# Performance work log

Measured on AMD Instinct MI355X. Metric: run time of the kernel, lower is better.

The kernel has to match this reference:

```python
import jax, jax.numpy as jnp
import numpy as np
from jax.scipy.special import erf, erfinv

N_OBS = 8192   # number of observations
N_LOC = 2048   # number of spatial locations (q)


def setup_inputs() -> dict:
    key = jax.random.key(0)
    k1, k2, k3, k4 = jax.random.split(key, 4)
    # random 2-D coordinates -> symmetric pairwise squared-distance matrix (zero diag)
    coords = jax.random.uniform(k1, (N_LOC, 2), dtype=jnp.float32) * 10.0
    dist_matrix = jnp.sum((coords[:, None, :] - coords[None, :, :]) ** 2, axis=-1)  # [q,q]
    Z_idx = jax.random.randint(k2, (N_OBS,), 0, N_LOC)                              # location id per obs
    y_true = jax.random.normal(k3, (N_OBS, 1), dtype=jnp.float32)
    y_pred = jax.random.normal(k4, (N_OBS, 1), dtype=jnp.float32) * 0.5
    return {
        "y_true": y_true,
        "y_pred": y_pred,
        "Z_idx": Z_idx,
        "dist_matrix": dist_matrix,
        "sig2e": jnp.array([1.0], dtype=jnp.float32),
        "sig2bs": jnp.array([0.5], dtype=jnp.float32),
        "lengthscale": jnp.array([2.0], dtype=jnp.float32),
    }


def _inverse_gaussian_cdf(u):
    # tf.math.erfinv(2*clip(u,1e-5,1-1e-5)-1) * sqrt(2)
    return erfinv(2.0 * jnp.clip(u, 1e-5, 1.0 - 1e-5) - 1.0) * jnp.sqrt(2.0)


def reference(y_true, y_pred, Z_idx, dist_matrix, sig2e, sig2bs, lengthscale):
    N = y_true.shape[0]
    q = dist_matrix.shape[0]
    dt = y_true.dtype
    # getD: exponential distance kernel over locations  D = sig2b * exp(-M / (2*ell))
    D = sig2bs[0] * jnp.exp(-dist_matrix / (2.0 * lengthscale[0]))          # [q,q]
    # getZ: dense one-hot design matrix (sparse.to_dense of SparseTensor of ones)
    Z = jax.nn.one_hot(Z_idx, q, dtype=dt)                                   # [N,q]
    # V_batch: V = Z D Z' + sig2e * I
    V = Z @ (D @ Z.T) + sig2e[0] * jnp.eye(N, dtype=dt)                      # [N,N]
    sd = jnp.sqrt(jnp.diagonal(V))                                           # sd_sqrt_V
    R = V / (sd[:, None] * sd[None, :])                                      # correlation matrix
    # Gaussian marginal: sig2 = sig2e + sig2b (diag of V)
    sig2 = sig2e[0] + sig2bs[0]
    resid = y_true - y_pred                                                  # [N,1]
    # distribution.cdf_batch: standard normal CDF of resid / sqrt(sig2)
    u = 0.5 * (erf(resid / jnp.sqrt(2.0 * sig2)) + 1.0)
    m = _inverse_gaussian_cdf(u)                                             # [N,1]
    # distribution.sum_log_pdf_batch: sum of Gaussian log-pdf
    sum_log_pdf = jnp.sum(-0.5 * jnp.log(2.0 * jnp.pi * sig2) - resid ** 2 / (2.0 * sig2))
    # solve + logdet via a single Cholesky of the correlation matrix
    L = jnp.linalg.cholesky(R)
    V_inv_m = jax.scipy.linalg.cho_solve((L, True), m)                       # R^{-1} m
    logdet = 2.0 * jnp.sum(jnp.log(jnp.diagonal(L)))                         # logdet(V) - 2*sum(log sd)
    mV_invm = m.T @ V_inv_m                                                  # [1,1]
    mtm = m.T @ m                                                            # [1,1]
    total_loss = 0.5 * logdet + 0.5 * mV_invm - 0.5 * mtm + 0.5 * sum_log_pdf
    return total_loss  # [1,1]
```

## Files before the change

kernel.cpp:

```cpp
#include <hip/hip_runtime.h>
#include <math.h>

#define Q 2048
#define NOBS 8192
#define NSTEPS 32

__device__ __forceinline__ float rl(float v, int l) {
  return __int_as_float(__builtin_amdgcn_readlane(__float_as_int(v), l));
}

__device__ __forceinline__ float block_sum256(float v, volatile float* red) {
  int tid = threadIdx.x;
#pragma unroll
  for (int o = 32; o > 0; o >>= 1) v += __shfl_down(v, o);
  __syncthreads();
  if ((tid & 63) == 0) red[tid >> 6] = v;
  __syncthreads();
  return red[0] + red[1] + red[2] + red[3];
}

__device__ __forceinline__ float chol64_reg(float rr[64], int lane) {
  float dv = 1.0f;
#pragma unroll
  for (int j = 0; j < 64; ++j) {
    float vjj = rl(rr[j], j);
    float invd = rsqrtf(vjj);
    float lij = rr[j] * invd;
    rr[j] = lij;
    if (lane == j) dv = lij;
#pragma unroll
    for (int k = j + 1; k < 64; ++k) rr[k] -= lij * rl(lij, k);
  }
  return dv;
}

__global__ __launch_bounds__(256) void obs_kernel(
    const float* __restrict__ yt, const float* __restrict__ yp,
    const int* __restrict__ zidx, const float* __restrict__ s2e_p,
    const float* __restrict__ s2b_p, float* __restrict__ t,
    int* __restrict__ cnt, float* __restrict__ scal) {
  __shared__ float red[4];
  int i = blockIdx.x * 256 + threadIdx.x;
  float s2e = s2e_p[0], s2b = s2b_p[0];
  float sig2 = s2e + s2b;
  float r = yt[i] - yp[i];
  float e = erff(r * rsqrtf(2.0f * sig2));
  float u = 0.5f * (e + 1.0f);
  u = fminf(fmaxf(u, 1e-5f), 1.0f - 1e-5f);
  float m = erfinvf(2.0f * u - 1.0f) * 1.4142135623730951f;
  float slp = -0.5f * logf(2.0f * 3.14159265358979f * sig2) - r * r / (2.0f * sig2);
  int z = zidx[i];
  atomicAdd(&t[z], m);
  atomicAdd(&cnt[z], 1);
  float s1 = block_sum256(slp, red);
  float s2 = block_sum256(m * m, red);
  if (threadIdx.x == 0) {
    atomicAdd(&scal[0], s1);
    atomicAdd(&scal[1], s2);
  }
}

__global__ __launch_bounds__(256) void build_G(
    const float* __restrict__ dist, const float* __restrict__ s2e_p,
    const float* __restrict__ s2b_p, const float* __restrict__ ell_p,
    const int* __restrict__ cnt, float* __restrict__ G) {
  int idx = blockIdx.x * 256 + threadIdx.x;
  int j = idx >> 11;
  int k = idx & (Q - 1);
  float s2e = s2e_p[0], s2b = s2b_p[0], ell = ell_p[0];
  float sig2 = s2e + s2b;
  float a = (s2b / sig2) * expf(-dist[idx] / (2.0f * ell));
  float g = sqrtf((float)cnt[j] * (float)cnt[k]) * a;
  if (j == k) g += s2e / sig2;
  G[idx] = g;
}

__global__ __launch_bounds__(256) void matvec_kernel(
    const float* __restrict__ dist, const float* __restrict__ s2e_p,
    const float* __restrict__ s2b_p, const float* __restrict__ ell_p,
    const int* __restrict__ cnt, const float* __restrict__ t,
    float* __restrict__ z, float* __restrict__ scal) {
  __shared__ float red[4];
  int j = blockIdx.x;
  float s2e = s2e_p[0], s2b = s2b_p[0], ell = ell_p[0];
  float sig2 = s2e + s2b;
  float inv2ell = 1.0f / (2.0f * ell);
  float s = 0.0f;
  const float* drow = dist + (size_t)j * Q;
  for (int k = threadIdx.x; k < Q; k += 256) s += expf(-drow[k] * inv2ell) * t[k];
  float tot = block_sum256(s, red);
  if (threadIdx.x == 0) {
    float wj = (s2b / sig2) * tot;
    z[j] = sqrtf((float)cnt[j]) * wj;
    atomicAdd(&scal[2], t[j] * wj);
  }
}

__global__ __launch_bounds__(64, 1) void potrf_first(
    const float* __restrict__ G, float* __restrict__ dstage,
    float* __restrict__ scal) {
  int lane = threadIdx.x;
  float rr[64];
  const float* row = G + (size_t)lane * Q;
#pragma unroll
  for (int k4 = 0; k4 < 16; ++k4) {
    float4 v = *(const float4*)(row + k4 * 4);
    rr[k4 * 4 + 0] = v.x; rr[k4 * 4 + 1] = v.y;
    rr[k4 * 4 + 2] = v.z; rr[k4 * 4 + 3] = v.w;
  }
  float dv = chol64_reg(rr, lane);
#pragma unroll
  for (int k4 = 0; k4 < 16; ++k4) {
    float4 st;
    st.x = rr[k4 * 4 + 0]; st.y = rr[k4 * 4 + 1];
    st.z = rr[k4 * 4 + 2]; st.w = rr[k4 * 4 + 3];
    *(float4*)(dstage + lane * 64 + k4 * 4) = st;
  }
  float lg = logf(dv);
#pragma unroll
  for (int o = 32; o > 0; o >>= 1) lg += __shfl_down(lg, o);
  if (lane == 0) atomicAdd(&scal[3], lg);
}

__global__ __launch_bounds__(256) void trsm_step(
    float* __restrict__ G, float* __restrict__ z,
    const float* __restrict__ dstage, int j0, int Rtot) {
  __shared__ float shA[64 * 65];
  int tid = threadIdx.x;
#pragma unroll
  for (int it = 0; it < 4; ++it) {
    int idx = it * 256 + tid;
    int r = idx >> 4, c = (idx & 15) * 4;
    float4 v = *(const float4*)(dstage + r * 64 + c);
    shA[r * 65 + c + 0] = v.x; shA[r * 65 + c + 1] = v.y;
    shA[r * 65 + c + 2] = v.z; shA[r * 65 + c + 3] = v.w;
  }
  __syncthreads();
  int lane = tid & 63, wv = tid >> 6;
  int ri = blockIdx.x * 4 + wv;
  if (ri >= Rtot) return;
  int r = j0 + 64 + ri;
  float* grow = (r < Q) ? (G + (size_t)r * Q + j0) : (z + j0);
  float a = grow[lane];
  float myinv = 1.0f / shA[lane * 65 + lane];
#pragma unroll
  for (int p = 0; p < 64; ++p) {
    float xp = rl(a, p) * rl(myinv, p);
    if (lane > p) a -= xp * shA[lane * 65 + p];
  }
  grow[lane] = a * myinv;
}

__device__ __forceinline__ void syrk_tile(float* __restrict__ G, int j0,
                                          int R0, int C0, float* shA,
                                          float* shB) {
  int tid = threadIdx.x;
#pragma unroll
  for (int it = 0; it < 4; ++it) {
    int idx = it * 256 + tid;
    int r = idx >> 4, c4 = (idx & 15) * 4;
    float4 v = *(const float4*)(G + (size_t)(R0 + r) * Q + j0 + c4);
    shA[(c4 + 0) * 68 + r] = v.x; shA[(c4 + 1) * 68 + r] = v.y;
    shA[(c4 + 2) * 68 + r] = v.z; shA[(c4 + 3) * 68 + r] = v.w;
    float4 u = *(const float4*)(G + (size_t)(C0 + r) * Q + j0 + c4);
    shB[(c4 + 0) * 68 + r] = u.x; shB[(c4 + 1) * 68 + r] = u.y;
    shB[(c4 + 2) * 68 + r] = u.z; shB[(c4 + 3) * 68 + r] = u.w;
  }
  __syncthreads();
  int tx = tid & 15, ty = tid >> 4;
  float acc[4][4] = {{0.f}};
  for (int p = 0; p < 64; ++p) {
    float4 a4 = *(const float4*)&shA[p * 68 + ty * 4];
    float4 b4 = *(const float4*)&shB[p * 68 + tx * 4];
    float av[4] = {a4.x, a4.y, a4.z, a4.w};
    float bv[4] = {b4.x, b4.y, b4.z, b4.w};
#pragma unroll
    for (int i = 0; i < 4; ++i)
#pragma unroll
      for (int jj = 0; jj < 4; ++jj) acc[i][jj] += av[i] * bv[jj];
  }
#pragma unroll
  for (int i = 0; i < 4; ++i) {
    float* gp = G + (size_t)(R0 + ty * 4 + i) * Q + C0 + tx * 4;
    float4 g = *(const float4*)gp;
    g.x -= acc[i][0]; g.y -= acc[i][1];
    g.z -= acc[i][2]; g.w -= acc[i][3];
    *(float4*)gp = g;
  }
}

__global__ __launch_bounds__(256, 1) void syrk_step(
    float* __restrict__ G, float* __restrict__ z, float* __restrict__ dstage,
    float* __restrict__ scal, int j0, int ntri) {
  __shared__ __align__(16) float shA[64 * 68];
  __shared__ __align__(16) float shB[64 * 68];
  __shared__ float z1s[64];
  int tid = threadIdx.x;
  int bx = blockIdx.x;

  if (bx == 0) {
    int D0 = j0 + 64;
#pragma unroll
    for (int it = 0; it < 4; ++it) {
      int idx = it * 256 + tid;
      int r2 = idx >> 4, c4 = (idx & 15) * 4;
      float4 v = *(const float4*)(G + (size_t)(D0 + r2) * Q + j0 + c4);
      shA[(c4 + 0) * 68 + r2] = v.x; shA[(c4 + 1) * 68 + r2] = v.y;
      shA[(c4 + 2) * 68 + r2] = v.z; shA[(c4 + 3) * 68 + r2] = v.w;
    }
    __syncthreads();
    int tx = tid & 15, ty = tid >> 4;
    float acc[4][4] = {{0.f}};
    for (int p = 0; p < 64; ++p) {
      float4 a4 = *(const float4*)&shA[p * 68 + ty * 4];
      float4 b4 = *(const float4*)&shA[p * 68 + tx * 4];
      float av[4] = {a4.x, a4.y, a4.z, a4.w};
      float bv[4] = {b4.x, b4.y, b4.z, b4.w};
#pragma unroll
      for (int i = 0; i < 4; ++i)
#pragma unroll
        for (int jj = 0; jj < 4; ++jj) acc[i][jj] += av[i] * bv[jj];
    }
#pragma unroll
    for (int i = 0; i < 4; ++i) {
      const float* gp = G + (size_t)(D0 + ty * 4 + i) * Q + D0 + tx * 4;
      float4 g = *(const float4*)gp;
      float4 o;
      o.x = g.x - acc[i][0]; o.y = g.y - acc[i][1];
      o.z = g.z - acc[i][2]; o.w = g.w - acc[i][3];
      *(float4*)&shB[(ty * 4 + i) * 68 + tx * 4] = o;
    }
    __syncthreads();
    if (tid < 64) {
      int lane = tid;
      float rr[64];
#pragma unroll
      for (int k4 = 0; k4 < 16; ++k4) {
        float4 v = *(const float4*)&shB[lane * 68 + k4 * 4];
        rr[k4 * 4 + 0] = v.x; rr[k4 * 4 + 1] = v.y;
        rr[k4 * 4 + 2] = v.z; rr[k4 * 4 + 3] = v.w;
      }
      __builtin_amdgcn_s_setprio(1);
      float dv = chol64_reg(rr, lane);
      __builtin_amdgcn_s_setprio(0);
#pragma unroll
      for (int k4 = 0; k4 < 16; ++k4) {
        float4 st;
        st.x = rr[k4 * 4 + 0]; st.y = rr[k4 * 4 + 1];
        st.z = rr[k4 * 4 + 2]; st.w = rr[k4 * 4 + 3];
        *(float4*)(dstage + lane * 64 + k4 * 4) = st;
      }
      float lg = logf(dv);
#pragma unroll
      for (int o = 32; o > 0; o >>= 1) lg += __shfl_down(lg, o);
      if (lane == 0) atomicAdd(&scal[3], lg);
    }
  } else if (bx < ntri) {
    int job = bx;
    int bi = (int)((sqrtf(8.0f * (float)job + 1.0f) - 1.0f) * 0.5f);
    while ((bi + 1) * (bi + 2) / 2 <= job) ++bi;
    while (bi * (bi + 1) / 2 > job) --bi;
    int bk = job - bi * (bi + 1) / 2;
    syrk_tile(G, j0, j0 + 64 + bi * 64, j0 + 64 + bk * 64, shA, shB);
  } else {
    int bk = bx - ntri;
    int C0 = j0 + 64 + bk * 64;
    if (tid < 64) z1s[tid] = z[j0 + tid];
    __syncthreads();
    int rw = tid >> 2, part = tid & 3;
    const float* Lr = G + (size_t)(C0 + rw) * Q + j0;
    float ssum = 0.f;
    for (int p = part; p < 64; p += 4) ssum += Lr[p] * z1s[p];
    ssum += __shfl_down(ssum, 2);
    ssum += __shfl_down(ssum, 1);
    if (part == 0) z[C0 + rw] -= ssum;
  }
}

__global__ __launch_bounds__(256) void final_assemble(
    const float* __restrict__ z, const float* __restrict__ scal,
    const float* __restrict__ s2e_p, const float* __restrict__ s2b_p,
    float* __restrict__ out) {
  __shared__ float red[4];
  int tid = threadIdx.x;
  float bv = 0.f;
  for (int i = tid; i < Q; i += 256) {
    float zi = z[i];
    bv += zi * zi;
  }
  float bvs = block_sum256(bv, red);
  if (tid == 0) {
    float s2e = s2e_p[0], s2b = s2b_p[0];
    float sig2 = s2e + s2b;
    float c = s2e / sig2;
    float slp = scal[0], mtm = scal[1];
    float tw = scal[2], sl = scal[3];
    float tty = (tw - bvs) / c;
    float mrm = (mtm - tty) / c;
    float logdetR = (float)(NOBS - Q) * logf(c) + 2.0f * sl;
    out[0] = 0.5f * logdetR + 0.5f * mrm - 0.5f * mtm + 0.5f * slp;
  }
}

extern "C" void kernel_launch(void* const* d_in, const int* in_sizes, int n_in,
                              void* d_out, int out_size, void* d_ws, size_t ws_size,
                              hipStream_t stream) {
  const float* yt   = (const float*)d_in[0];
  const float* yp   = (const float*)d_in[1];
  const int*   zidx = (const int*)d_in[2];
  const float* dist = (const float*)d_in[3];
  const float* s2e  = (const float*)d_in[4];
  const float* s2b  = (const float*)d_in[5];
  const float* ell  = (const float*)d_in[6];

  float* ws   = (float*)d_ws;
  float* G    = ws;
  float* z    = ws + (size_t)Q * Q;
  float* t    = z + Q;
  int*   cnt  = (int*)(t + Q);
  float* scal = t + 2 * Q;
  float* dstage = scal + 8;

  hipMemsetAsync(t, 0, (2 * Q + 8) * sizeof(float), stream);

  obs_kernel<<<NOBS / 256, 256, 0, stream>>>(yt, yp, zidx, s2e, s2b, t, cnt, scal);
  build_G<<<(Q * Q) / 256, 256, 0, stream>>>(dist, s2e, s2b, ell, cnt, G);
  matvec_kernel<<<Q, 256, 0, stream>>>(dist, s2e, s2b, ell, cnt, t, z, scal);

  potrf_first<<<1, 64, 0, stream>>>(G, dstage, scal);

  for (int s = 0; s < NSTEPS; ++s) {
    int j0 = s * 64;
    int ntr = Q - j0 - 64;
    int Rtot = ntr + 1;
    int nb = ntr >> 6;
    trsm_step<<<(Rtot + 3) / 4, 256, 0, stream>>>(G, z, dstage, j0, Rtot);
    if (nb > 0) {
      int ntri = nb * (nb + 1) / 2;
      syrk_step<<<ntri + nb, 256, 0, stream>>>(G, z, dstage, scal, j0, ntri);
    }
  }

  final_assemble<<<1, 256, 0, stream>>>(z, scal, s2e, s2b, (float*)d_out);
}
```

Measured before the change: 886.8 us.

## Use 128-wide panels in blocked Cholesky with 8x8 register tiles and fused G build

```diff
diff --git a/kernel.cpp b/kernel.cpp
--- a/kernel.cpp
+++ b/kernel.cpp
@@ -3,7 +3,8 @@
 
 #define Q 2048
 #define NOBS 8192
-#define NSTEPS 32
+#define BS 128
+#define NSTEPS 16
 
 __device__ __forceinline__ float rl(float v, int l) {
   return __int_as_float(__builtin_amdgcn_readlane(__float_as_int(v), l));
@@ -32,6 +33,136 @@
     for (int k = j + 1; k < 64; ++k) rr[k] -= lij * rl(lij, k);
   }
   return dv;
+}
+
+__device__ __forceinline__ void factor128_from(
+    const float* src, int sstride, float* dstage,
+    float* LT, float* Xs, float* invDs, float* scal) {
+  int tid = threadIdx.x;
+  int lane = tid & 63;
+  float lg = 0.0f;
+
+  if (tid < 64) {
+    float rr[64];
+    const float* row = src + (size_t)lane * sstride;
+#pragma unroll
+    for (int k4 = 0; k4 < 16; ++k4) {
+      float4 v = *(const float4*)(row + k4 * 4);
+      rr[k4 * 4 + 0] = v.x; rr[k4 * 4 + 1] = v.y;
+      rr[k4 * 4 + 2] = v.z; rr[k4 * 4 + 3] = v.w;
+    }
+    __builtin_amdgcn_s_setprio(1);
+    float dv = chol64_reg(rr, lane);
+    __builtin_amdgcn_s_setprio(0);
+    invDs[lane] = 1.0f / dv;
+    lg = logf(dv);
+#pragma unroll
+    for (int p = 0; p < 64; ++p)
+      LT[p * 64 + lane] = (p < lane) ? rr[p] : 0.0f;
+#pragma unroll
+    for (int k4 = 0; k4 < 16; ++k4) {
+      float4 st;
+      st.x = rr[k4 * 4 + 0]; st.y = rr[k4 * 4 + 1];
+      st.z = rr[k4 * 4 + 2]; st.w = rr[k4 * 4 + 3];
+      *(float4*)(dstage + lane * 128 + k4 * 4) = st;
+    }
+  }
+  __syncthreads();
+
+  if (tid < 64) {
+    float rr2[64];
+    const float* row = src + (size_t)(64 + lane) * sstride;
+#pragma unroll
+    for (int k4 = 0; k4 < 16; ++k4) {
+      float4 v = *(const float4*)(row + k4 * 4);
+      rr2[k4 * 4 + 0] = v.x; rr2[k4 * 4 + 1] = v.y;
+      rr2[k4 * 4 + 2] = v.z; rr2[k4 * 4 + 3] = v.w;
+    }
+    __builtin_amdgcn_s_setprio(1);
+#pragma unroll
+    for (int p = 0; p < 64; ++p) {
+      float xp = rr2[p] * invDs[p];
+      rr2[p] = xp;
+#pragma unroll
+      for (int k4 = 0; k4 < 16; ++k4) {
+        if (k4 * 4 + 3 > p) {
+          float4 l4 = *(const float4*)&LT[p * 64 + k4 * 4];
+          rr2[k4 * 4 + 0] -= xp * l4.x;
+          rr2[k4 * 4 + 1] -= xp * l4.y;
+          rr2[k4 * 4 + 2] -= xp * l4.z;
+          rr2[k4 * 4 + 3] -= xp * l4.w;
+        }
+      }
+    }
+    __builtin_amdgcn_s_setprio(0);
+#pragma unroll
+    for (int k = 0; k < 64; ++k) Xs[lane * 65 + k] = rr2[k];
+#pragma unroll
+    for (int k4 = 0; k4 < 16; ++k4) {
+      float4 st;
+      st.x = rr2[k4 * 4 + 0]; st.y = rr2[k4 * 4 + 1];
+      st.z = rr2[k4 * 4 + 2]; st.w = rr2[k4 * 4 + 3];
+      *(float4*)(dstage + (64 + lane) * 128 + k4 * 4) = st;
+    }
+  }
+  __syncthreads();
+
+  {
+    int tx = tid & 15, ty = tid >> 4;
+    float a2[4][4];
+#pragma unroll
+    for (int i = 0; i < 4; ++i)
+#pragma unroll
+      for (int j = 0; j < 4; ++j) a2[i][j] = 0.f;
+    for (int p = 0; p < 64; ++p) {
+      float xa[4], xb[4];
+#pragma unroll
+      for (int i = 0; i < 4; ++i) xa[i] = Xs[(ty * 4 + i) * 65 + p];
+#pragma unroll
+      for (int j = 0; j < 4; ++j) xb[j] = Xs[(tx * 4 + j) * 65 + p];
+#pragma unroll
+      for (int i = 0; i < 4; ++i)
+#pragma unroll
+        for (int j = 0; j < 4; ++j) a2[i][j] += xa[i] * xb[j];
+    }
+#pragma unroll
+    for (int i = 0; i < 4; ++i) {
+      int gr = 64 + ty * 4 + i;
+      const float* sp = src + (size_t)gr * sstride + 64 + tx * 4;
+      float4 s4 = *(const float4*)sp;
+      float4 o;
+      o.x = s4.x - a2[i][0]; o.y = s4.y - a2[i][1];
+      o.z = s4.z - a2[i][2]; o.w = s4.w - a2[i][3];
+      *(float4*)(dstage + gr * 128 + 64 + tx * 4) = o;
+    }
+  }
+  __syncthreads();
+  __builtin_amdgcn_fence(__ATOMIC_ACQUIRE, "workgroup");
+
+  if (tid < 64) {
+    float rr3[64];
+    const float* row = dstage + (64 + lane) * 128 + 64;
+#pragma unroll
+    for (int k4 = 0; k4 < 16; ++k4) {
+      float4 v = *(const float4*)(row + k4 * 4);
+      rr3[k4 * 4 + 0] = v.x; rr3[k4 * 4 + 1] = v.y;
+      rr3[k4 * 4 + 2] = v.z; rr3[k4 * 4 + 3] = v.w;
+    }
+    __builtin_amdgcn_s_setprio(1);
+    float dv = chol64_reg(rr3, lane);
+    __builtin_amdgcn_s_setprio(0);
+    lg += logf(dv);
+#pragma unroll
+    for (int k4 = 0; k4 < 16; ++k4) {
+      float4 st;
+      st.x = rr3[k4 * 4 + 0]; st.y = rr3[k4 * 4 + 1];
+      st.z = rr3[k4 * 4 + 2]; st.w = rr3[k4 * 4 + 3];
+      *(float4*)(dstage + (64 + lane) * 128 + 64 + k4 * 4) = st;
+    }
+#pragma unroll
+    for (int o = 32; o > 0; o >>= 1) lg += __shfl_down(lg, o);
+    if (lane == 0) atomicAdd(&scal[3], lg);
+  }
 }
 
 __global__ __launch_bounds__(256) void obs_kernel(
@@ -60,220 +191,210 @@
   }
 }
 
-__global__ __launch_bounds__(256) void build_G(
-    const float* __restrict__ dist, const float* __restrict__ s2e_p,
-    const float* __restrict__ s2b_p, const float* __restrict__ ell_p,
-    const int* __restrict__ cnt, float* __restrict__ G) {
-  int idx = blockIdx.x * 256 + threadIdx.x;
-  int j = idx >> 11;
-  int k = idx & (Q - 1);
-  float s2e = s2e_p[0], s2b = s2b_p[0], ell = ell_p[0];
-  float sig2 = s2e + s2b;
-  float a = (s2b / sig2) * expf(-dist[idx] / (2.0f * ell));
-  float g = sqrtf((float)cnt[j] * (float)cnt[k]) * a;
-  if (j == k) g += s2e / sig2;
-  G[idx] = g;
-}
-
-__global__ __launch_bounds__(256) void matvec_kernel(
+__global__ __launch_bounds__(256) void build_mv(
     const float* __restrict__ dist, const float* __restrict__ s2e_p,
     const float* __restrict__ s2b_p, const float* __restrict__ ell_p,
     const int* __restrict__ cnt, const float* __restrict__ t,
-    float* __restrict__ z, float* __restrict__ scal) {
+    float* __restrict__ G, float* __restrict__ z, float* __restrict__ scal) {
   __shared__ float red[4];
   int j = blockIdx.x;
   float s2e = s2e_p[0], s2b = s2b_p[0], ell = ell_p[0];
   float sig2 = s2e + s2b;
+  float ratio = s2b / sig2;
+  float diag = s2e / sig2;
   float inv2ell = 1.0f / (2.0f * ell);
+  float cj = (float)cnt[j];
+  const float* drow = dist + (size_t)j * Q;
+  float* grow = G + (size_t)j * Q;
   float s = 0.0f;
-  const float* drow = dist + (size_t)j * Q;
-  for (int k = threadIdx.x; k < Q; k += 256) s += expf(-drow[k] * inv2ell) * t[k];
+  for (int k = threadIdx.x; k < Q; k += 256) {
+    float e = expf(-drow[k] * inv2ell);
+    s += e * t[k];
+    float g = sqrtf(cj * (float)cnt[k]) * (ratio * e);
+    if (j == k) g += diag;
+    grow[k] = g;
+  }
   float tot = block_sum256(s, red);
   if (threadIdx.x == 0) {
-    float wj = (s2b / sig2) * tot;
-    z[j] = sqrtf((float)cnt[j]) * wj;
+    float wj = ratio * tot;
+    z[j] = sqrtf(cj) * wj;
     atomicAdd(&scal[2], t[j] * wj);
   }
 }
 
-__global__ __launch_bounds__(64, 1) void potrf_first(
+__global__ __launch_bounds__(256, 1) void potrf_first(
     const float* __restrict__ G, float* __restrict__ dstage,
     float* __restrict__ scal) {
-  int lane = threadIdx.x;
-  float rr[64];
-  const float* row = G + (size_t)lane * Q;
-#pragma unroll
-  for (int k4 = 0; k4 < 16; ++k4) {
-    float4 v = *(const float4*)(row + k4 * 4);
-    rr[k4 * 4 + 0] = v.x; rr[k4 * 4 + 1] = v.y;
-    rr[k4 * 4 + 2] = v.z; rr[k4 * 4 + 3] = v.w;
-  }
-  float dv = chol64_reg(rr, lane);
-#pragma unroll
-  for (int k4 = 0; k4 < 16; ++k4) {
-    float4 st;
-    st.x = rr[k4 * 4 + 0]; st.y = rr[k4 * 4 + 1];
-    st.z = rr[k4 * 4 + 2]; st.w = rr[k4 * 4 + 3];
-    *(float4*)(dstage + lane * 64 + k4 * 4) = st;
-  }
-  float lg = logf(dv);
-#pragma unroll
-  for (int o = 32; o > 0; o >>= 1) lg += __shfl_down(lg, o);
-  if (lane == 0) atomicAdd(&scal[3], lg);
+  __shared__ __align__(16) float smem[64 * 64 + 64 * 65];
+  __shared__ float invDs[64];
+  factor128_from(G, Q, dstage, smem, smem + 64 * 64, invDs, scal);
 }
 
 __global__ __launch_bounds__(256) void trsm_step(
     float* __restrict__ G, float* __restrict__ z,
     const float* __restrict__ dstage, int j0, int Rtot) {
-  __shared__ float shA[64 * 65];
+  __shared__ float shL[128 * 129];
   int tid = threadIdx.x;
 #pragma unroll
-  for (int it = 0; it < 4; ++it) {
+  for (int it = 0; it < 16; ++it) {
     int idx = it * 256 + tid;
-    int r = idx >> 4, c = (idx & 15) * 4;
-    float4 v = *(const float4*)(dstage + r * 64 + c);
-    shA[r * 65 + c + 0] = v.x; shA[r * 65 + c + 1] = v.y;
-    shA[r * 65 + c + 2] = v.z; shA[r * 65 + c + 3] = v.w;
+    int r = idx >> 5, c4 = (idx & 31) * 4;
+    float4 v = *(const float4*)(dstage + r * 128 + c4);
+    shL[r * 129 + c4 + 0] = v.x; shL[r * 129 + c4 + 1] = v.y;
+    shL[r * 129 + c4 + 2] = v.z; shL[r * 129 + c4 + 3] = v.w;
   }
   __syncthreads();
   int lane = tid & 63, wv = tid >> 6;
   int ri = blockIdx.x * 4 + wv;
   if (ri >= Rtot) return;
-  int r = j0 + 64 + ri;
+  int r = j0 + BS + ri;
   float* grow = (r < Q) ? (G + (size_t)r * Q + j0) : (z + j0);
-  float a = grow[lane];
-  float myinv = 1.0f / shA[lane * 65 + lane];
+  float a0 = grow[lane];
+  float a1 = grow[64 + lane];
+  float inv0 = 1.0f / shL[lane * 129 + lane];
+  float inv1 = 1.0f / shL[(64 + lane) * 129 + 64 + lane];
 #pragma unroll
   for (int p = 0; p < 64; ++p) {
-    float xp = rl(a, p) * rl(myinv, p);
-    if (lane > p) a -= xp * shA[lane * 65 + p];
-  }
-  grow[lane] = a * myinv;
-}
-
-__device__ __forceinline__ void syrk_tile(float* __restrict__ G, int j0,
-                                          int R0, int C0, float* shA,
-                                          float* shB) {
-  int tid = threadIdx.x;
-#pragma unroll
-  for (int it = 0; it < 4; ++it) {
-    int idx = it * 256 + tid;
-    int r = idx >> 4, c4 = (idx & 15) * 4;
-    float4 v = *(const float4*)(G + (size_t)(R0 + r) * Q + j0 + c4);
-    shA[(c4 + 0) * 68 + r] = v.x; shA[(c4 + 1) * 68 + r] = v.y;
-    shA[(c4 + 2) * 68 + r] = v.z; shA[(c4 + 3) * 68 + r] = v.w;
-    float4 u = *(const float4*)(G + (size_t)(C0 + r) * Q + j0 + c4);
-    shB[(c4 + 0) * 68 + r] = u.x; shB[(c4 + 1) * 68 + r] = u.y;
-    shB[(c4 + 2) * 68 + r] = u.z; shB[(c4 + 3) * 68 + r] = u.w;
-  }
-  __syncthreads();
-  int tx = tid & 15, ty = tid >> 4;
-  float acc[4][4] = {{0.f}};
+    float xp = rl(a0, p) * rl(inv0, p);
+    if (lane > p) a0 -= xp * shL[lane * 129 + p];
+    a1 -= xp * shL[(64 + lane) * 129 + p];
+  }
+#pragma unroll
   for (int p = 0; p < 64; ++p) {
-    float4 a4 = *(const float4*)&shA[p * 68 + ty * 4];
-    float4 b4 = *(const float4*)&shB[p * 68 + tx * 4];
-    float av[4] = {a4.x, a4.y, a4.z, a4.w};
-    float bv[4] = {b4.x, b4.y, b4.z, b4.w};
-#pragma unroll
-    for (int i = 0; i < 4; ++i)
-#pragma unroll
-      for (int jj = 0; jj < 4; ++jj) acc[i][jj] += av[i] * bv[jj];
-  }
-#pragma unroll
-  for (int i = 0; i < 4; ++i) {
-    float* gp = G + (size_t)(R0 + ty * 4 + i) * Q + C0 + tx * 4;
-    float4 g = *(const float4*)gp;
-    g.x -= acc[i][0]; g.y -= acc[i][1];
-    g.z -= acc[i][2]; g.w -= acc[i][3];
-    *(float4*)gp = g;
-  }
+    float xp = rl(a1, p) * rl(inv1, p);
+    if (lane > p) a1 -= xp * shL[(64 + lane) * 129 + 64 + p];
+  }
+  grow[lane] = a0 * inv0;
+  grow[64 + lane] = a1 * inv1;
 }
 
 __global__ __launch_bounds__(256, 1) void syrk_step(
     float* __restrict__ G, float* __restrict__ z, float* __restrict__ dstage,
-    float* __restrict__ scal, int j0, int ntri) {
-  __shared__ __align__(16) float shA[64 * 68];
-  __shared__ __align__(16) float shB[64 * 68];
-  __shared__ float z1s[64];
+    float* __restrict__ scal, int j0, int ntri, int nb) {
+  __shared__ __align__(16) float smem[2 * 32 * 132];
+  __shared__ float invDs[64];
+  __shared__ float z1s[128];
   int tid = threadIdx.x;
   int bx = blockIdx.x;
+  float* shA = smem;
+  float* shB = smem + 32 * 132;
+
+  if (bx >= ntri) {
+    int zj = bx - ntri;
+    int C0 = j0 + BS + zj * BS;
+    if (tid < 128) z1s[tid] = z[j0 + tid];
+    __syncthreads();
+    int rw = tid >> 1, part = tid & 1;
+    const float* Lr = G + (size_t)(C0 + rw) * Q + j0;
+    float ssum = 0.f;
+    for (int p = part; p < 128; p += 2) ssum += Lr[p] * z1s[p];
+    ssum += __shfl_down(ssum, 1);
+    if (part == 0) z[C0 + rw] -= ssum;
+    return;
+  }
+
+  int tx = tid & 15, ty = tid >> 4;
+  float acc[8][8];
+#pragma unroll
+  for (int i = 0; i < 8; ++i)
+#pragma unroll
+    for (int j = 0; j < 8; ++j) acc[i][j] = 0.f;
 
   if (bx == 0) {
-    int D0 = j0 + 64;
+    int D0 = j0 + BS;
+    for (int kk = 0; kk < 4; ++kk) {
+#pragma unroll
+      for (int it = 0; it < 4; ++it) {
+        int idx = it * 256 + tid;
+        int r = idx >> 3, c4 = (idx & 7) * 4;
+        float4 v = *(const float4*)(G + (size_t)(D0 + r) * Q + j0 + kk * 32 + c4);
+        shA[(c4 + 0) * 132 + r] = v.x; shA[(c4 + 1) * 132 + r] = v.y;
+        shA[(c4 + 2) * 132 + r] = v.z; shA[(c4 + 3) * 132 + r] = v.w;
+      }
+      __syncthreads();
+#pragma unroll
+      for (int p = 0; p < 32; ++p) {
+        float4 a0 = *(const float4*)&shA[p * 132 + ty * 8];
+        float4 a1 = *(const float4*)&shA[p * 132 + ty * 8 + 4];
+        float4 b0 = *(const float4*)&shA[p * 132 + tx * 8];
+        float4 b1 = *(const float4*)&shA[p * 132 + tx * 8 + 4];
+        float av[8] = {a0.x, a0.y, a0.z, a0.w, a1.x, a1.y, a1.z, a1.w};
+        float bv[8] = {b0.x, b0.y, b0.z, b0.w, b1.x, b1.y, b1.z, b1.w};
+#pragma unroll
+        for (int i = 0; i < 8; ++i)
+#pragma unroll
+          for (int j = 0; j < 8; ++j) acc[i][j] += av[i] * bv[j];
+      }
+      __syncthreads();
+    }
+#pragma unroll
+    for (int i = 0; i < 8; ++i) {
+      const float* gp = G + (size_t)(D0 + ty * 8 + i) * Q + D0 + tx * 8;
+      float4 g0 = *(const float4*)gp;
+      float4 g1 = *(const float4*)(gp + 4);
+      float4 o0, o1;
+      o0.x = g0.x - acc[i][0]; o0.y = g0.y - acc[i][1];
+      o0.z = g0.z - acc[i][2]; o0.w = g0.w - acc[i][3];
+      o1.x = g1.x - acc[i][4]; o1.y = g1.y - acc[i][5];
+      o1.z = g1.z - acc[i][6]; o1.w = g1.w - acc[i][7];
+      *(float4*)(dstage + (ty * 8 + i) * 128 + tx * 8) = o0;
+      *(float4*)(dstage + (ty * 8 + i) * 128 + tx * 8 + 4) = o1;
+    }
+    __syncthreads();
+    __builtin_amdgcn_fence(__ATOMIC_ACQUIRE, "workgroup");
+    factor128_from(dstage, 128, dstage, smem, smem + 64 * 64, invDs, scal);
+    return;
+  }
+
+  int job = bx;
+  int bi = (int)((sqrtf(8.0f * (float)job + 1.0f) - 1.0f) * 0.5f);
+  while ((bi + 1) * (bi + 2) / 2 <= job) ++bi;
+  while (bi * (bi + 1) / 2 > job) --bi;
+  int bk = job - bi * (bi + 1) / 2;
+  int R0 = j0 + BS + bi * BS;
+  int C0 = j0 + BS + bk * BS;
+  bool sym = (bi == bk);
+
+  for (int kk = 0; kk < 4; ++kk) {
 #pragma unroll
     for (int it = 0; it < 4; ++it) {
       int idx = it * 256 + tid;
-      int r2 = idx >> 4, c4 = (idx & 15) * 4;
-      float4 v = *(const float4*)(G + (size_t)(D0 + r2) * Q + j0 + c4);
-      shA[(c4 + 0) * 68 + r2] = v.x; shA[(c4 + 1) * 68 + r2] = v.y;
-      shA[(c4 + 2) * 68 + r2] = v.z; shA[(c4 + 3) * 68 + r2] = v.w;
+      int r = idx >> 3, c4 = (idx & 7) * 4;
+      float4 v = *(const float4*)(G + (size_t)(R0 + r) * Q + j0 + kk * 32 + c4);
+      shA[(c4 + 0) * 132 + r] = v.x; shA[(c4 + 1) * 132 + r] = v.y;
+      shA[(c4 + 2) * 132 + r] = v.z; shA[(c4 + 3) * 132 + r] = v.w;
+      if (!sym) {
+        float4 u = *(const float4*)(G + (size_t)(C0 + r) * Q + j0 + kk * 32 + c4);
+        shB[(c4 + 0) * 132 + r] = u.x; shB[(c4 + 1) * 132 + r] = u.y;
+        shB[(c4 + 2) * 132 + r] = u.z; shB[(c4 + 3) * 132 + r] = u.w;
+      }
     }
     __syncthreads();
-    int tx = tid & 15, ty = tid >> 4;
-    float acc[4][4] = {{0.f}};
-    for (int p = 0; p < 64; ++p) {
-      float4 a4 = *(const float4*)&shA[p * 68 + ty * 4];
-      float4 b4 = *(const float4*)&shA[p * 68 + tx * 4];
-      float av[4] = {a4.x, a4.y, a4.z, a4.w};
-      float bv[4] = {b4.x, b4.y, b4.z, b4.w};
-#pragma unroll
-      for (int i = 0; i < 4; ++i)
-#pragma unroll
-        for (int jj = 0; jj < 4; ++jj) acc[i][jj] += av[i] * bv[jj];
-    }
-#pragma unroll
-    for (int i = 0; i < 4; ++i) {
-      const float* gp = G + (size_t)(D0 + ty * 4 + i) * Q + D0 + tx * 4;
-      float4 g = *(const float4*)gp;
-      float4 o;
-      o.x = g.x - acc[i][0]; o.y = g.y - acc[i][1];
-      o.z = g.z - acc[i][2]; o.w = g.w - acc[i][3];
-      *(float4*)&shB[(ty * 4 + i) * 68 + tx * 4] = o;
+    const float* sB = sym ? shA : shB;
+#pragma unroll
+    for (int p = 0; p < 32; ++p) {
+      float4 a0 = *(const float4*)&shA[p * 132 + ty * 8];
+      float4 a1 = *(const float4*)&shA[p * 132 + ty * 8 + 4];
+      float4 b0 = *(const float4*)&sB[p * 132 + tx * 8];
+      float4 b1 = *(const float4*)&sB[p * 132 + tx * 8 + 4];
+      float av[8] = {a0.x, a0.y, a0.z, a0.w, a1.x, a1.y, a1.z, a1.w};
+      float bv[8] = {b0.x, b0.y, b0.z, b0.w, b1.x, b1.y, b1.z, b1.w};
+#pragma unroll
+      for (int i = 0; i < 8; ++i)
+#pragma unroll
+        for (int j = 0; j < 8; ++j) acc[i][j] += av[i] * bv[j];
     }
     __syncthreads();
-    if (tid < 64) {
-      int lane = tid;
-      float rr[64];
-#pragma unroll
-      for (int k4 = 0; k4 < 16; ++k4) {
-        float4 v = *(const float4*)&shB[lane * 68 + k4 * 4];
-        rr[k4 * 4 + 0] = v.x; rr[k4 * 4 + 1] = v.y;
-        rr[k4 * 4 + 2] = v.z; rr[k4 * 4 + 3] = v.w;
-      }
-      __builtin_amdgcn_s_setprio(1);
-      float dv = chol64_reg(rr, lane);
-      __builtin_amdgcn_s_setprio(0);
-#pragma unroll
-      for (int k4 = 0; k4 < 16; ++k4) {
-        float4 st;
-        st.x = rr[k4 * 4 + 0]; st.y = rr[k4 * 4 + 1];
-        st.z = rr[k4 * 4 + 2]; st.w = rr[k4 * 4 + 3];
-        *(float4*)(dstage + lane * 64 + k4 * 4) = st;
-      }
-      float lg = logf(dv);
-#pragma unroll
-      for (int o = 32; o > 0; o >>= 1) lg += __shfl_down(lg, o);
-      if (lane == 0) atomicAdd(&scal[3], lg);
-    }
-  } else if (bx < ntri) {
-    int job = bx;
-    int bi = (int)((sqrtf(8.0f * (float)job + 1.0f) - 1.0f) * 0.5f);
-    while ((bi + 1) * (bi + 2) / 2 <= job) ++bi;
-    while (bi * (bi + 1) / 2 > job) --bi;
-    int bk = job - bi * (bi + 1) / 2;
-    syrk_tile(G, j0, j0 + 64 + bi * 64, j0 + 64 + bk * 64, shA, shB);
-  } else {
-    int bk = bx - ntri;
-    int C0 = j0 + 64 + bk * 64;
-    if (tid < 64) z1s[tid] = z[j0 + tid];
-    __syncthreads();
-    int rw = tid >> 2, part = tid & 3;
-    const float* Lr = G + (size_t)(C0 + rw) * Q + j0;
-    float ssum = 0.f;
-    for (int p = part; p < 64; p += 4) ssum += Lr[p] * z1s[p];
-    ssum += __shfl_down(ssum, 2);
-    ssum += __shfl_down(ssum, 1);
-    if (part == 0) z[C0 + rw] -= ssum;
+  }
+#pragma unroll
+  for (int i = 0; i < 8; ++i) {
+    float* gp = G + (size_t)(R0 + ty * 8 + i) * Q + C0 + tx * 8;
+    float4 g0 = *(const float4*)gp;
+    float4 g1 = *(const float4*)(gp + 4);
+    g0.x -= acc[i][0]; g0.y -= acc[i][1]; g0.z -= acc[i][2]; g0.w -= acc[i][3];
+    g1.x -= acc[i][4]; g1.y -= acc[i][5]; g1.z -= acc[i][6]; g1.w -= acc[i][7];
+    *(float4*)gp = g0;
+    *(float4*)(gp + 4) = g1;
   }
 }
 
@@ -324,20 +445,19 @@
   hipMemsetAsync(t, 0, (2 * Q + 8) * sizeof(float), stream);
 
   obs_kernel<<<NOBS / 256, 256, 0, stream>>>(yt, yp, zidx, s2e, s2b, t, cnt, scal);
-  build_G<<<(Q * Q) / 256, 256, 0, stream>>>(dist, s2e, s2b, ell, cnt, G);
-  matvec_kernel<<<Q, 256, 0, stream>>>(dist, s2e, s2b, ell, cnt, t, z, scal);
-
-  potrf_first<<<1, 64, 0, stream>>>(G, dstage, scal);
+  build_mv<<<Q, 256, 0, stream>>>(dist, s2e, s2b, ell, cnt, t, G, z, scal);
+
+  potrf_first<<<1, 256, 0, stream>>>(G, dstage, scal);
 
   for (int s = 0; s < NSTEPS; ++s) {
-    int j0 = s * 64;
-    int ntr = Q - j0 - 64;
+    int j0 = s * BS;
+    int ntr = Q - j0 - BS;
     int Rtot = ntr + 1;
-    int nb = ntr >> 6;
+    int nb = ntr / BS;
     trsm_step<<<(Rtot + 3) / 4, 256, 0, stream>>>(G, z, dstage, j0, Rtot);
     if (nb > 0) {
       int ntri = nb * (nb + 1) / 2;
-      syrk_step<<<ntri + nb, 256, 0, stream>>>(G, z, dstage, scal, j0, ntri);
+      syrk_step<<<ntri + nb, 256, 0, stream>>>(G, z, dstage, scal, j0, ntri, nb);
     }
   }
 
```

After: 1.188 ms. 34.0% more time.

## Fuse TRSM and SYRK per step with flag-based intra-kernel dependencies

Applied to the files above, without the earlier changes.

```diff
diff --git a/kernel.cpp b/kernel.cpp
--- a/kernel.cpp
+++ b/kernel.cpp
@@ -3,7 +3,6 @@
 
 #define Q 2048
 #define NOBS 8192
-#define NSTEPS 32
 
 __device__ __forceinline__ float rl(float v, int l) {
   return __int_as_float(__builtin_amdgcn_readlane(__float_as_int(v), l));
@@ -32,6 +31,12 @@
     for (int k = j + 1; k < 64; ++k) rr[k] -= lij * rl(lij, k);
   }
   return dv;
+}
+
+__device__ __forceinline__ void wait_flag(int* f, int target) {
+  while (__hip_atomic_load(f, __ATOMIC_RELAXED, __HIP_MEMORY_SCOPE_AGENT) <
+         target)
+    __builtin_amdgcn_s_sleep(8);
 }
 
 __global__ __launch_bounds__(256) void obs_kernel(
@@ -60,45 +65,40 @@
   }
 }
 
-__global__ __launch_bounds__(256) void build_G(
-    const float* __restrict__ dist, const float* __restrict__ s2e_p,
-    const float* __restrict__ s2b_p, const float* __restrict__ ell_p,
-    const int* __restrict__ cnt, float* __restrict__ G) {
-  int idx = blockIdx.x * 256 + threadIdx.x;
-  int j = idx >> 11;
-  int k = idx & (Q - 1);
-  float s2e = s2e_p[0], s2b = s2b_p[0], ell = ell_p[0];
-  float sig2 = s2e + s2b;
-  float a = (s2b / sig2) * expf(-dist[idx] / (2.0f * ell));
-  float g = sqrtf((float)cnt[j] * (float)cnt[k]) * a;
-  if (j == k) g += s2e / sig2;
-  G[idx] = g;
-}
-
-__global__ __launch_bounds__(256) void matvec_kernel(
+__global__ __launch_bounds__(256) void build_mv(
     const float* __restrict__ dist, const float* __restrict__ s2e_p,
     const float* __restrict__ s2b_p, const float* __restrict__ ell_p,
     const int* __restrict__ cnt, const float* __restrict__ t,
-    float* __restrict__ z, float* __restrict__ scal) {
+    float* __restrict__ G, float* __restrict__ z, float* __restrict__ scal) {
   __shared__ float red[4];
   int j = blockIdx.x;
   float s2e = s2e_p[0], s2b = s2b_p[0], ell = ell_p[0];
   float sig2 = s2e + s2b;
+  float ratio = s2b / sig2;
+  float diag = s2e / sig2;
   float inv2ell = 1.0f / (2.0f * ell);
+  float cj = (float)cnt[j];
+  const float* drow = dist + (size_t)j * Q;
+  float* grow = G + (size_t)j * Q;
   float s = 0.0f;
-  const float* drow = dist + (size_t)j * Q;
-  for (int k = threadIdx.x; k < Q; k += 256) s += expf(-drow[k] * inv2ell) * t[k];
+  for (int k = threadIdx.x; k < Q; k += 256) {
+    float e = expf(-drow[k] * inv2ell);
+    s += e * t[k];
+    float g = sqrtf(cj * (float)cnt[k]) * (ratio * e);
+    if (j == k) g += diag;
+    grow[k] = g;
+  }
   float tot = block_sum256(s, red);
   if (threadIdx.x == 0) {
-    float wj = (s2b / sig2) * tot;
-    z[j] = sqrtf((float)cnt[j]) * wj;
+    float wj = ratio * tot;
+    z[j] = sqrtf(cj) * wj;
     atomicAdd(&scal[2], t[j] * wj);
   }
 }
 
 __global__ __launch_bounds__(64, 1) void potrf_first(
-    const float* __restrict__ G, float* __restrict__ dstage,
-    float* __restrict__ scal) {
+    const float* __restrict__ G, float* __restrict__ dsA,
+    float* __restrict__ z, float* __restrict__ scal) {
   int lane = threadIdx.x;
   float rr[64];
   const float* row = G + (size_t)lane * Q;
@@ -114,92 +114,85 @@
     float4 st;
     st.x = rr[k4 * 4 + 0]; st.y = rr[k4 * 4 + 1];
     st.z = rr[k4 * 4 + 2]; st.w = rr[k4 * 4 + 3];
-    *(float4*)(dstage + lane * 64 + k4 * 4) = st;
+    *(float4*)(dsA + lane * 64 + k4 * 4) = st;
   }
   float lg = logf(dv);
 #pragma unroll
   for (int o = 32; o > 0; o >>= 1) lg += __shfl_down(lg, o);
   if (lane == 0) atomicAdd(&scal[3], lg);
-}
-
-__global__ __launch_bounds__(256) void trsm_step(
-    float* __restrict__ G, float* __restrict__ z,
-    const float* __restrict__ dstage, int j0, int Rtot) {
-  __shared__ float shA[64 * 65];
-  int tid = threadIdx.x;
-#pragma unroll
-  for (int it = 0; it < 4; ++it) {
-    int idx = it * 256 + tid;
-    int r = idx >> 4, c = (idx & 15) * 4;
-    float4 v = *(const float4*)(dstage + r * 64 + c);
-    shA[r * 65 + c + 0] = v.x; shA[r * 65 + c + 1] = v.y;
-    shA[r * 65 + c + 2] = v.z; shA[r * 65 + c + 3] = v.w;
-  }
-  __syncthreads();
-  int lane = tid & 63, wv = tid >> 6;
-  int ri = blockIdx.x * 4 + wv;
-  if (ri >= Rtot) return;
-  int r = j0 + 64 + ri;
-  float* grow = (r < Q) ? (G + (size_t)r * Q + j0) : (z + j0);
-  float a = grow[lane];
-  float myinv = 1.0f / shA[lane * 65 + lane];
+  float a = z[lane];
+  float myinv = 1.0f / dv;
 #pragma unroll
   for (int p = 0; p < 64; ++p) {
     float xp = rl(a, p) * rl(myinv, p);
-    if (lane > p) a -= xp * shA[lane * 65 + p];
-  }
-  grow[lane] = a * myinv;
-}
-
-__device__ __forceinline__ void syrk_tile(float* __restrict__ G, int j0,
-                                          int R0, int C0, float* shA,
-                                          float* shB) {
-  int tid = threadIdx.x;
-#pragma unroll
-  for (int it = 0; it < 4; ++it) {
-    int idx = it * 256 + tid;
-    int r = idx >> 4, c4 = (idx & 15) * 4;
-    float4 v = *(const float4*)(G + (size_t)(R0 + r) * Q + j0 + c4);
-    shA[(c4 + 0) * 68 + r] = v.x; shA[(c4 + 1) * 68 + r] = v.y;
-    shA[(c4 + 2) * 68 + r] = v.z; shA[(c4 + 3) * 68 + r] = v.w;
-    float4 u = *(const float4*)(G + (size_t)(C0 + r) * Q + j0 + c4);
-    shB[(c4 + 0) * 68 + r] = u.x; shB[(c4 + 1) * 68 + r] = u.y;
-    shB[(c4 + 2) * 68 + r] = u.z; shB[(c4 + 3) * 68 + r] = u.w;
-  }
-  __syncthreads();
-  int tx = tid & 15, ty = tid >> 4;
-  float acc[4][4] = {{0.f}};
-  for (int p = 0; p < 64; ++p) {
-    float4 a4 = *(const float4*)&shA[p * 68 + ty * 4];
-    float4 b4 = *(const float4*)&shB[p * 68 + tx * 4];
-    float av[4] = {a4.x, a4.y, a4.z, a4.w};
-    float bv[4] = {b4.x, b4.y, b4.z, b4.w};
-#pragma unroll
-    for (int i = 0; i < 4; ++i)
-#pragma unroll
-      for (int jj = 0; jj < 4; ++jj) acc[i][jj] += av[i] * bv[jj];
-  }
-#pragma unroll
-  for (int i = 0; i < 4; ++i) {
-    float* gp = G + (size_t)(R0 + ty * 4 + i) * Q + C0 + tx * 4;
-    float4 g = *(const float4*)gp;
-    g.x -= acc[i][0]; g.y -= acc[i][1];
-    g.z -= acc[i][2]; g.w -= acc[i][3];
-    *(float4*)gp = g;
-  }
-}
-
-__global__ __launch_bounds__(256, 1) void syrk_step(
-    float* __restrict__ G, float* __restrict__ z, float* __restrict__ dstage,
-    float* __restrict__ scal, int j0, int ntri) {
-  __shared__ __align__(16) float shA[64 * 68];
-  __shared__ __align__(16) float shB[64 * 68];
+    if (lane > p) a -= xp * rr[p];
+  }
+  z[lane] = a * myinv;
+}
+
+__global__ __launch_bounds__(256, 2) void step_kernel(
+    float* __restrict__ G, float* __restrict__ z, float* __restrict__ scal,
+    const float* __restrict__ dsR, float* __restrict__ dsW,
+    int* __restrict__ flags, int j0, int ntri, int n64, int T, int mode) {
+  __shared__ __align__(16) float smem[2 * 64 * 68];
   __shared__ float z1s[64];
-  int tid = threadIdx.x;
-  int bx = blockIdx.x;
+  __shared__ float z2s[64];
+  float* shA = smem;
+  float* shB = smem + 64 * 68;
+  int tid = threadIdx.x, bx = blockIdx.x;
+  int lane = tid & 63, wv = tid >> 6;
+  int s1 = (j0 >> 6) + 1;
+  int D0 = j0 + 64;
+  int ztop = ntri + n64 - 1;
+
+  if (mode == 1 || (mode == 0 && bx >= ztop)) {
+    int t = (mode == 1) ? bx : bx - ztop;
+#pragma unroll
+    for (int it = 0; it < 4; ++it) {
+      int idx = it * 256 + tid;
+      int r = idx >> 4, c = (idx & 15) * 4;
+      float4 v = *(const float4*)(dsR + r * 64 + c);
+      shA[r * 65 + c + 0] = v.x; shA[r * 65 + c + 1] = v.y;
+      shA[r * 65 + c + 2] = v.z; shA[r * 65 + c + 3] = v.w;
+    }
+    __syncthreads();
+    int rbase = D0 + t * 16 + wv * 4;
+    float* g0 = G + (size_t)(rbase + 0) * Q + j0;
+    float* g1 = G + (size_t)(rbase + 1) * Q + j0;
+    float* g2 = G + (size_t)(rbase + 2) * Q + j0;
+    float* g3 = G + (size_t)(rbase + 3) * Q + j0;
+    float a0 = g0[lane], a1 = g1[lane], a2 = g2[lane], a3 = g3[lane];
+    float myinv = 1.0f / shA[lane * 65 + lane];
+#pragma unroll
+    for (int p = 0; p < 64; ++p) {
+      float ip = rl(myinv, p);
+      float x0 = rl(a0, p) * ip;
+      float x1 = rl(a1, p) * ip;
+      float x2 = rl(a2, p) * ip;
+      float x3 = rl(a3, p) * ip;
+      float lv = shA[lane * 65 + p];
+      if (lane > p) {
+        a0 -= x0 * lv; a1 -= x1 * lv; a2 -= x2 * lv; a3 -= x3 * lv;
+      }
+    }
+    g0[lane] = a0 * myinv; g1[lane] = a1 * myinv;
+    g2[lane] = a2 * myinv; g3[lane] = a3 * myinv;
+    __syncthreads();
+    if (tid == 0) {
+      __builtin_amdgcn_fence(__ATOMIC_RELEASE, "agent");
+      __hip_atomic_fetch_add(&flags[s1 + (t >> 2)], 1, __ATOMIC_RELAXED,
+                             __HIP_MEMORY_SCOPE_AGENT);
+    }
+    return;
+  }
 
   if (bx == 0) {
-    int D0 = j0 + 64;
+    if (tid == 0) {
+      wait_flag(&flags[s1], T);
+      __builtin_amdgcn_fence(__ATOMIC_ACQUIRE, "agent");
+    }
+    __syncthreads();
+    if (tid < 64) z1s[tid] = z[j0 + tid];
 #pragma unroll
     for (int it = 0; it < 4; ++it) {
       int idx = it * 256 + tid;
@@ -221,6 +214,14 @@
 #pragma unroll
         for (int jj = 0; jj < 4; ++jj) acc[i][jj] += av[i] * bv[jj];
     }
+    {
+      int rw = tid >> 2, part = tid & 3;
+      float ssum = 0.f;
+      for (int p = part; p < 64; p += 4) ssum += shA[p * 68 + rw] * z1s[p];
+      ssum += __shfl_down(ssum, 2);
+      ssum += __shfl_down(ssum, 1);
+      if (part == 0) z2s[rw] = z[D0 + rw] - ssum;
+    }
 #pragma unroll
     for (int i = 0; i < 4; ++i) {
       const float* gp = G + (size_t)(D0 + ty * 4 + i) * Q + D0 + tx * 4;
@@ -232,7 +233,6 @@
     }
     __syncthreads();
     if (tid < 64) {
-      int lane = tid;
       float rr[64];
 #pragma unroll
       for (int k4 = 0; k4 < 16; ++k4) {
@@ -248,25 +248,86 @@
         float4 st;
         st.x = rr[k4 * 4 + 0]; st.y = rr[k4 * 4 + 1];
         st.z = rr[k4 * 4 + 2]; st.w = rr[k4 * 4 + 3];
-        *(float4*)(dstage + lane * 64 + k4 * 4) = st;
+        *(float4*)(dsW + lane * 64 + k4 * 4) = st;
       }
       float lg = logf(dv);
 #pragma unroll
       for (int o = 32; o > 0; o >>= 1) lg += __shfl_down(lg, o);
       if (lane == 0) atomicAdd(&scal[3], lg);
-    }
-  } else if (bx < ntri) {
+      float a = z2s[lane];
+      float myinv = 1.0f / dv;
+#pragma unroll
+      for (int p = 0; p < 64; ++p) {
+        float xp = rl(a, p) * rl(myinv, p);
+        if (lane > p) a -= xp * rr[p];
+      }
+      z[D0 + lane] = a * myinv;
+    }
+    return;
+  }
+
+  if (bx < ntri) {
     int job = bx;
     int bi = (int)((sqrtf(8.0f * (float)job + 1.0f) - 1.0f) * 0.5f);
     while ((bi + 1) * (bi + 2) / 2 <= job) ++bi;
     while (bi * (bi + 1) / 2 > job) --bi;
     int bk = job - bi * (bi + 1) / 2;
-    syrk_tile(G, j0, j0 + 64 + bi * 64, j0 + 64 + bk * 64, shA, shB);
-  } else {
-    int bk = bx - ntri;
-    int C0 = j0 + 64 + bk * 64;
+    if (tid == 0) {
+      wait_flag(&flags[s1 + bi], T);
+      if (bk != bi) wait_flag(&flags[s1 + bk], T);
+      __builtin_amdgcn_fence(__ATOMIC_ACQUIRE, "agent");
+    }
+    __syncthreads();
+    int R0 = D0 + bi * 64, C0 = D0 + bk * 64;
+    bool sym = (bi == bk);
+#pragma unroll
+    for (int it = 0; it < 4; ++it) {
+      int idx = it * 256 + tid;
+      int r = idx >> 4, c4 = (idx & 15) * 4;
+      float4 v = *(const float4*)(G + (size_t)(R0 + r) * Q + j0 + c4);
+      shA[(c4 + 0) * 68 + r] = v.x; shA[(c4 + 1) * 68 + r] = v.y;
+      shA[(c4 + 2) * 68 + r] = v.z; shA[(c4 + 3) * 68 + r] = v.w;
+      if (!sym) {
+        float4 u = *(const float4*)(G + (size_t)(C0 + r) * Q + j0 + c4);
+        shB[(c4 + 0) * 68 + r] = u.x; shB[(c4 + 1) * 68 + r] = u.y;
+        shB[(c4 + 2) * 68 + r] = u.z; shB[(c4 + 3) * 68 + r] = u.w;
+      }
+    }
+    __syncthreads();
+    const float* sB = sym ? shA : shB;
+    int tx = tid & 15, ty = tid >> 4;
+    float acc[4][4] = {{0.f}};
+    for (int p = 0; p < 64; ++p) {
+      float4 a4 = *(const float4*)&shA[p * 68 + ty * 4];
+      float4 b4 = *(const float4*)&sB[p * 68 + tx * 4];
+      float av[4] = {a4.x, a4.y, a4.z, a4.w};
+      float bv[4] = {b4.x, b4.y, b4.z, b4.w};
+#pragma unroll
+      for (int i = 0; i < 4; ++i)
+#pragma unroll
+        for (int jj = 0; jj < 4; ++jj) acc[i][jj] += av[i] * bv[jj];
+    }
+#pragma unroll
+    for (int i = 0; i < 4; ++i) {
+      float* gp = G + (size_t)(R0 + ty * 4 + i) * Q + C0 + tx * 4;
+      float4 g = *(const float4*)gp;
+      g.x -= acc[i][0]; g.y -= acc[i][1];
+      g.z -= acc[i][2]; g.w -= acc[i][3];
+      *(float4*)gp = g;
+    }
+    return;
+  }
+
+  {
+    int bk = bx - ntri + 1;
+    if (tid == 0) {
+      wait_flag(&flags[s1 + bk], T);
+      __builtin_amdgcn_fence(__ATOMIC_ACQUIRE, "agent");
+    }
+    __syncthreads();
     if (tid < 64) z1s[tid] = z[j0 + tid];
     __syncthreads();
+    int C0 = D0 + bk * 64;
     int rw = tid >> 2, part = tid & 3;
     const float* Lr = G + (size_t)(C0 + rw) * Q + j0;
     float ssum = 0.f;
@@ -317,27 +378,35 @@
   float* G    = ws;
   float* z    = ws + (size_t)Q * Q;
   float* t    = z + Q;
-  int*   cnt  = (int*)(t + Q);
+  int*   cntv = (int*)(t + Q);
   float* scal = t + 2 * Q;
-  float* dstage = scal + 8;
-
-  hipMemsetAsync(t, 0, (2 * Q + 8) * sizeof(float), stream);
-
-  obs_kernel<<<NOBS / 256, 256, 0, stream>>>(yt, yp, zidx, s2e, s2b, t, cnt, scal);
-  build_G<<<(Q * Q) / 256, 256, 0, stream>>>(dist, s2e, s2b, ell, cnt, G);
-  matvec_kernel<<<Q, 256, 0, stream>>>(dist, s2e, s2b, ell, cnt, t, z, scal);
-
-  potrf_first<<<1, 64, 0, stream>>>(G, dstage, scal);
-
-  for (int s = 0; s < NSTEPS; ++s) {
+  int*   flags = (int*)(scal + 8);
+  float* dsA  = scal + 8 + 64;
+  float* dsB  = dsA + 4096;
+
+  hipMemsetAsync(t, 0, (2 * Q + 8 + 64) * sizeof(float), stream);
+
+  obs_kernel<<<NOBS / 256, 256, 0, stream>>>(yt, yp, zidx, s2e, s2b, t, cntv, scal);
+  build_mv<<<Q, 256, 0, stream>>>(dist, s2e, s2b, ell, cntv, t, G, z, scal);
+
+  potrf_first<<<1, 64, 0, stream>>>(G, dsA, z, scal);
+
+  for (int s = 0; s < 31; ++s) {
+    int n64 = 31 - s;
+    int ntri = n64 * (n64 + 1) / 2;
     int j0 = s * 64;
-    int ntr = Q - j0 - 64;
-    int Rtot = ntr + 1;
-    int nb = ntr >> 6;
-    trsm_step<<<(Rtot + 3) / 4, 256, 0, stream>>>(G, z, dstage, j0, Rtot);
-    if (nb > 0) {
-      int ntri = nb * (nb + 1) / 2;
-      syrk_step<<<ntri + nb, 256, 0, stream>>>(G, z, dstage, scal, j0, ntri);
+    int T = 4 * (s + 1);
+    float* dsR = (s & 1) ? dsB : dsA;
+    float* dsW = (s & 1) ? dsA : dsB;
+    int gfull = ntri + 5 * n64 - 1;
+    if (gfull <= 512) {
+      step_kernel<<<gfull, 256, 0, stream>>>(G, z, scal, dsR, dsW, flags,
+                                             j0, ntri, n64, T, 0);
+    } else {
+      step_kernel<<<4 * n64, 256, 0, stream>>>(G, z, scal, dsR, dsW, flags,
+                                               j0, ntri, n64, T, 1);
+      step_kernel<<<ntri + n64 - 1, 256, 0, stream>>>(G, z, scal, dsR, dsW,
+                                                      flags, j0, ntri, n64, T, 2);
     }
   }
 
```

Result: slower. 1.038 ms (+17.0%).
